# Optimization experiments

Measured on AMD Instinct MI355X. Metric: run time of the kernel, lower is better.

The kernel has to match this reference:

```python
import jax, jax.numpy as jnp
import numpy as np

C = 128      # input_dim
HEADS = 1    # inner_dim == input_dim (required by W_o channel counts)
INNER = C * HEADS
H = W = 80
EPS = 1e-5


def conv1x1(x, w, b):
    # x: [1,Cin,H,W], w: [Cout,Cin], b: [Cout]
    return jnp.einsum('bchw,oc->bohw', x, w) + b[None, :, None, None]


def bn_train(x, gamma, beta):
    # train-mode BatchNorm2d: per-channel stats over (B,H,W)
    mean = jnp.mean(x, axis=(0, 2, 3), keepdims=True)
    var = jnp.var(x, axis=(0, 2, 3), keepdims=True)
    xn = (x - mean) * jax.lax.rsqrt(var + EPS)
    return gamma[None, :, None, None] * xn + beta[None, :, None, None]


def proj(x, w, b, g, bt):
    return jax.nn.relu(bn_train(conv1x1(x, w, b), g, bt))


def setup_inputs() -> dict:
    key = jax.random.key(0)
    ks = jax.random.split(key, 12)
    d = {
        'query': jax.random.normal(ks[0], (1, C, H, W), jnp.float32),
        'key': jax.random.normal(ks[1], (1, C, H, W), jnp.float32),
        'value': jax.random.normal(ks[2], (1, C, H, W), jnp.float32),
        'pos_embedding': jax.random.normal(ks[3], (1, H, W), jnp.float32),
    }
    def lin(k, co, ci):
        return jax.random.normal(k, (co, ci), jnp.float32) * 0.02
    for name, k in zip(['q', 'k', 'v'], ks[4:7]):
        d['w' + name] = lin(k, INNER, C)
        d['b' + name] = jnp.zeros((INNER,), jnp.float32)
        d['g' + name] = jnp.ones((INNER,), jnp.float32)
        d['beta' + name] = jnp.zeros((INNER,), jnp.float32)
    d['wo1'] = lin(ks[7], C, INNER)
    d['bo1'] = jnp.zeros((C,), jnp.float32)
    d['go'] = jnp.ones((C,), jnp.float32)
    d['betao'] = jnp.zeros((C,), jnp.float32)
    d['wo2'] = lin(ks[8], C, INNER)
    d['bo2'] = jnp.zeros((C,), jnp.float32)
    return d


def reference(query, key, value, pos_embedding,
              wq, bq, gq, betaq,
              wk, bk, gk, betak,
              wv, bv, gv, betav,
              wo1, bo1, go, betao, wo2, bo2):
    dim = query.shape[1]
    q = proj(query, wq, bq, gq, betaq)   # [1,INNER,H,W]
    k = proj(key, wk, bk, gk, betak)
    v = proj(value, wv, bv, gv, betav)
    N = q.shape[2] * q.shape[3]
    # heads=1: rearrange 'b (c h) x y -> b h (x y) c' == flatten+transpose
    q2 = q.reshape(INNER, N).T           # [N, INNER]
    k2 = k.reshape(INNER, N).T
    v2 = v.reshape(INNER, N).T
    # pos context: pos repeated across all channels -> q2 @ ctx^T is an outer product
    pos = pos_embedding.reshape(N)
    ctx = jnp.sum(q2, axis=-1, keepdims=True) * pos[None, :]   # [N, N]
    score = (q2 @ k2.T) / jnp.sqrt(jnp.float32(dim)) + ctx
    attn = jax.nn.softmax(score, axis=-1)
    out = attn @ v2                      # [N, INNER]
    # buggy original rearrange: x = N, y = 1 -> spatial [N, 1]
    out = out.T.reshape(1, INNER, N, 1)
    h = jax.nn.relu(bn_train(conv1x1(out, wo1, bo1), go, betao))
    return conv1x1(h, wo2, bo2)          # [1, C, N, 1]
```

## Files before the change

### kernel.cpp

```cpp
#include <hip/hip_runtime.h>

#define NPIX 6400

typedef float f4 __attribute__((ext_vector_type(4)));
typedef float f16v __attribute__((ext_vector_type(16)));
typedef short bf16x8 __attribute__((ext_vector_type(8)));
typedef unsigned int u4 __attribute__((ext_vector_type(4)));
typedef unsigned int u2 __attribute__((ext_vector_type(2)));
typedef _Float16 h8 __attribute__((ext_vector_type(8)));
typedef _Float16 h4 __attribute__((ext_vector_type(4)));
typedef unsigned short u16;
typedef unsigned int u32;

__device__ __forceinline__ u16 f2bf(float f){
  union { float f; u32 u; } v; v.f = f;
  u32 r = v.u + 0x7fffu + ((v.u >> 16) & 1u);
  return (u16)(r >> 16);
}
__device__ __forceinline__ float bf2f(u16 h){
  union { u32 u; float f; } v; v.u = (u32)h << 16; return v.f;
}
__device__ __forceinline__ float exp2_hw(float x){ return __builtin_amdgcn_exp2f(x); }

__global__ __launch_bounds__(512, 1) void k_proj(
    const float* __restrict__ xq, const float* __restrict__ xk, const float* __restrict__ xv,
    const float* __restrict__ wq, const float* __restrict__ bq,
    const float* __restrict__ wk, const float* __restrict__ bk,
    const float* __restrict__ wv, const float* __restrict__ bv,
    u16* __restrict__ Y, float* __restrict__ psum, float* __restrict__ psq)
{
  __shared__ __align__(16) float wT[64][132];
  __shared__ __align__(16) float xt[64][132];
  __shared__ __align__(16) float red[2][16][128];
  const int bid = blockIdx.x;
  const int proj = bid / 50, pt = bid % 50;
  const float* x = (proj == 0) ? xq : ((proj == 1) ? xk : xv);
  const float* w = (proj == 0) ? wq : ((proj == 1) ? wk : wv);
  const float* b = (proj == 0) ? bq : ((proj == 1) ? bk : bv);
  const int t = threadIdx.x;
  const int o0 = (t & 31) * 4, p0 = (t >> 5) * 8;
  float acc[4][8];
  #pragma unroll
  for (int i = 0; i < 4; ++i)
    #pragma unroll
    for (int j = 0; j < 8; ++j) acc[i][j] = 0.f;
  for (int cc = 0; cc < 2; ++cc){
    __syncthreads();
    for (int idx = t; idx < 2048; idx += 512){
      int o = idx >> 4, c4 = (idx & 15) * 4;
      f4 wv4 = *(const f4*)&w[o * 128 + cc * 64 + c4];
      wT[c4 + 0][o] = wv4[0]; wT[c4 + 1][o] = wv4[1];
      wT[c4 + 2][o] = wv4[2]; wT[c4 + 3][o] = wv4[3];
    }
    for (int idx = t; idx < 2048; idx += 512){
      int c = idx >> 5, p4 = (idx & 31) * 4;
      *(f4*)&xt[c][p4] = *(const f4*)&x[(cc * 64 + c) * NPIX + pt * 128 + p4];
    }
    __syncthreads();
    for (int c = 0; c < 64; ++c){
      f4 w4 = *(const f4*)&wT[c][o0];
      f4 x0 = *(const f4*)&xt[c][p0];
      f4 x1 = *(const f4*)&xt[c][p0 + 4];
      #pragma unroll
      for (int i = 0; i < 4; ++i){
        float wi = w4[i];
        #pragma unroll
        for (int j = 0; j < 4; ++j){ acc[i][j] += wi * x0[j]; acc[i][4 + j] += wi * x1[j]; }
      }
    }
  }
  f4 b4 = *(const f4*)&b[o0];
  #pragma unroll
  for (int i = 0; i < 4; ++i)
    #pragma unroll
    for (int j = 0; j < 8; ++j) acc[i][j] += b4[i];
  #pragma unroll
  for (int i = 0; i < 4; ++i){
    float s = 0.f, q = 0.f;
    #pragma unroll
    for (int j = 0; j < 8; ++j){ s += acc[i][j]; q += acc[i][j] * acc[i][j]; }
    red[0][t >> 5][o0 + i] = s;
    red[1][t >> 5][o0 + i] = q;
  }
  __syncthreads();
  if (t < 128){
    float s = 0.f, q = 0.f;
    #pragma unroll
    for (int g = 0; g < 16; ++g){ s += red[0][g][t]; q += red[1][g][t]; }
    psum[(proj * 50 + pt) * 128 + t] = s;
    psq [(proj * 50 + pt) * 128 + t] = q;
  }
  u16* Yb = Y + (size_t)proj * NPIX * 128;
  if (proj < 2){
    #pragma unroll
    for (int j = 0; j < 8; ++j){
      u2 v;
      v[0] = (u32)f2bf(acc[0][j]) | ((u32)f2bf(acc[1][j]) << 16);
      v[1] = (u32)f2bf(acc[2][j]) | ((u32)f2bf(acc[3][j]) << 16);
      *(u2*)&Yb[(size_t)(pt * 128 + p0 + j) * 128 + o0] = v;
    }
  } else {
    #pragma unroll
    for (int i = 0; i < 4; ++i){
      u4 v;
      #pragma unroll
      for (int jj = 0; jj < 4; ++jj)
        v[jj] = (u32)f2bf(acc[i][jj * 2]) | ((u32)f2bf(acc[i][jj * 2 + 1]) << 16);
      *(u4*)&Yb[(size_t)(o0 + i) * NPIX + pt * 128 + p0] = v;
    }
  }
}

__global__ __launch_bounds__(512, 1) void k_norm(
    const u16* __restrict__ Y, const float* __restrict__ psum, const float* __restrict__ psq,
    const float* __restrict__ gq, const float* __restrict__ beq,
    const float* __restrict__ gk, const float* __restrict__ bek,
    const float* __restrict__ gv, const float* __restrict__ bev,
    u16* __restrict__ q2, u16* __restrict__ k2, u16* __restrict__ v2t,
    float* __restrict__ rowsumq)
{
  __shared__ float sc[128], sh[128];
  const int bid = blockIdx.x, t = threadIdx.x;
  const int proj = bid / 50, pt = bid % 50;
  if (t < 128){
    float s = 0.f, q = 0.f;
    for (int i = 0; i < 50; ++i){
      s += psum[(proj * 50 + i) * 128 + t];
      q += psq [(proj * 50 + i) * 128 + t];
    }
    float mean = s * (1.f / NPIX);
    float var  = q * (1.f / NPIX) - mean * mean;
    const float* g  = (proj == 0) ? gq : ((proj == 1) ? gk : gv);
    const float* be = (proj == 0) ? beq : ((proj == 1) ? bek : bev);
    float scale = g[t] * rsqrtf(var + 1e-5f);
    sc[t] = scale; sh[t] = be[t] - mean * scale;
  }
  __syncthreads();
  const u16* Yb = Y + (size_t)proj * NPIX * 128;
  if (proj < 2){
    int row = pt * 128 + (t >> 2), o0 = (t & 3) * 32;
    float rs = 0.f;
    u32 pkd[16];
    #pragma unroll
    for (int u = 0; u < 4; ++u){
      bf16x8 y8 = *(const bf16x8*)&Yb[(size_t)row * 128 + o0 + u * 8];
      #pragma unroll
      for (int e = 0; e < 8; ++e){
        int o = o0 + u * 8 + e;
        float v = fmaxf(bf2f((u16)y8[e]) * sc[o] + sh[o], 0.f);
        rs += v;
        if ((e & 1) == 0) pkd[u * 4 + (e >> 1)] = (u32)f2bf(v);
        else pkd[u * 4 + (e >> 1)] |= ((u32)f2bf(v) << 16);
      }
    }
    u16* dst = (proj == 0) ? q2 : k2;
    u4* dp = (u4*)(dst + (size_t)row * 128 + o0);
    #pragma unroll
    for (int u = 0; u < 4; ++u){
      u4 v; v[0] = pkd[u*4]; v[1] = pkd[u*4+1]; v[2] = pkd[u*4+2]; v[3] = pkd[u*4+3];
      dp[u] = v;
    }
    if (proj == 0){
      rs += __shfl_xor(rs, 1);
      rs += __shfl_xor(rs, 2);
      if ((t & 3) == 0) rowsumq[row] = rs;
    }
  } else {
    int o = t >> 2, pc = pt * 128 + (t & 3) * 32;
    float scale = sc[o], shift = sh[o];
    u32 pkd[16];
    #pragma unroll
    for (int u = 0; u < 4; ++u){
      bf16x8 y8 = *(const bf16x8*)&Yb[(size_t)o * NPIX + pc + u * 8];
      #pragma unroll
      for (int e = 0; e < 8; ++e){
        float v = fmaxf(bf2f((u16)y8[e]) * scale + shift, 0.f);
        if ((e & 1) == 0) pkd[u * 4 + (e >> 1)] = (u32)f2bf(v);
        else pkd[u * 4 + (e >> 1)] |= ((u32)f2bf(v) << 16);
      }
    }
    u4* dp = (u4*)(v2t + (size_t)o * NPIX + pc);
    #pragma unroll
    for (int u = 0; u < 4; ++u){
      u4 v; v[0] = pkd[u*4]; v[1] = pkd[u*4+1]; v[2] = pkd[u*4+2]; v[3] = pkd[u*4+3];
      dp[u] = v;
    }
  }
}

template<int NKT>
__global__ __launch_bounds__(512, 2) void k_flash(
    const u16* __restrict__ q2, const u16* __restrict__ k2, const u16* __restrict__ v2t,
    const float* __restrict__ rowsumq, const float* __restrict__ pos,
    _Float16* __restrict__ Opart, float* __restrict__ Mout, float* __restrict__ Lout,
    int js)
{
  __shared__ __align__(16) u16 Kt[2][64 * 128];
  __shared__ __align__(16) u16 Vt[2][128 * 64];
  __shared__ __align__(16) float posT[2][64];
  const int bid = blockIdx.x;
  const int qb = bid / js, jsi = bid % js;
  const int kt0 = jsi * NKT;
  const int tid = threadIdx.x;
  const int ln = tid & 63, wid = tid >> 6;
  const int lo = ln & 31, hi = ln >> 5;
  const int qrow = qb * 256 + wid * 32 + lo;

  const int kc_j = tid >> 4, kc_c8 = tid & 15;
  const int vc_d = tid >> 3, vc_c8 = tid & 7;
  bf16x8 kreg0, kreg1, vreg0, vreg1; float posr = 0.f;
  auto stage_load = [&](int j0){
    kreg0 = *(const bf16x8*)(k2 + (size_t)(j0 + kc_j) * 128 + kc_c8 * 8);
    kreg1 = *(const bf16x8*)(k2 + (size_t)(j0 + kc_j + 32) * 128 + kc_c8 * 8);
    vreg0 = *(const bf16x8*)(v2t + (size_t)vc_d * NPIX + j0 + vc_c8 * 8);
    vreg1 = *(const bf16x8*)(v2t + (size_t)(vc_d + 64) * NPIX + j0 + vc_c8 * 8);
    if (tid < 64) posr = pos[j0 + tid];
  };
  auto stage_write = [&](int b){
    char* kb = (char*)&Kt[b][0];
    char* vb = (char*)&Vt[b][0];
    *(bf16x8*)(kb + kc_j * 256 + ((kc_c8 * 16) ^ ((kc_j & 15) << 4))) = kreg0;
    *(bf16x8*)(kb + (kc_j + 32) * 256 + ((kc_c8 * 16) ^ (((kc_j + 32) & 15) << 4))) = kreg1;
    *(bf16x8*)(vb + vc_d * 128 + ((vc_c8 * 16) ^ ((vc_d & 7) << 4))) = vreg0;
    *(bf16x8*)(vb + (vc_d + 64) * 128 + ((vc_c8 * 16) ^ (((vc_d + 64) & 7) << 4))) = vreg1;
    if (tid < 64) posT[b][tid] = posr;
  };

  bf16x8 qf[8];
  const u16* qp = q2 + (size_t)qrow * 128 + hi * 8;
  #pragma unroll
  for (int kk = 0; kk < 8; ++kk) qf[kk] = *(const bf16x8*)(qp + kk * 16);
  const float rsq_l2 = rowsumq[qrow] * 1.4426950408889634f;
  f16v accO[4];
  #pragma unroll
  for (int c = 0; c < 4; ++c)
    #pragma unroll
    for (int r = 0; r < 16; ++r) accO[c][r] = 0.f;
  float m = -1e30f, l = 0.f;
  const float qs_l2 = 0.12751700f;

  stage_load(kt0 * 64);
  stage_write(0);
  __syncthreads();
  int cur = 0;

  #pragma unroll 2
  for (int kt = 0; kt < NKT; ++kt){
    const bool more = (kt + 1 < NKT);
    if (more) stage_load((kt0 + kt + 1) * 64);

    f16v aS0a, aS0b, aS1a, aS1b;
    #pragma unroll
    for (int r = 0; r < 16; ++r){ aS0a[r] = 0.f; aS0b[r] = 0.f; aS1a[r] = 0.f; aS1b[r] = 0.f; }
    {
      const char* kb0 = (const char*)&Kt[cur][0] + lo * 256;
      const char* kb1 = (const char*)&Kt[cur][0] + (32 + lo) * 256;
      const int sw = (lo & 15) << 4;
      #pragma unroll
      for (int kk = 0; kk < 4; ++kk){
        int boA = (kk * 32 + hi * 16) ^ sw;
        int boB = ((kk + 4) * 32 + hi * 16) ^ sw;
        bf16x8 kf0a = *(const bf16x8*)(kb0 + boA);
        bf16x8 kf1a = *(const bf16x8*)(kb1 + boA);
        bf16x8 kf0b = *(const bf16x8*)(kb0 + boB);
        bf16x8 kf1b = *(const bf16x8*)(kb1 + boB);
        aS0a = __builtin_amdgcn_mfma_f32_32x32x16_bf16(kf0a, qf[kk], aS0a, 0, 0, 0);
        aS1a = __builtin_amdgcn_mfma_f32_32x32x16_bf16(kf1a, qf[kk], aS1a, 0, 0, 0);
        aS0b = __builtin_amdgcn_mfma_f32_32x32x16_bf16(kf0b, qf[kk + 4], aS0b, 0, 0, 0);
        aS1b = __builtin_amdgcn_mfma_f32_32x32x16_bf16(kf1b, qf[kk + 4], aS1b, 0, 0, 0);
      }
    }
    float pv[32];
    float mx = -1e30f;
    #pragma unroll
    for (int jsb = 0; jsb < 2; ++jsb){
      #pragma unroll
      for (int g = 0; g < 4; ++g){
        f4 p4 = *(const f4*)&posT[cur][jsb * 32 + g * 8 + hi * 4];
        #pragma unroll
        for (int e = 0; e < 4; ++e){
          float sraw = jsb ? (aS1a[g * 4 + e] + aS1b[g * 4 + e])
                           : (aS0a[g * 4 + e] + aS0b[g * 4 + e]);
          float sv = sraw * qs_l2 + rsq_l2 * p4[e];
          pv[jsb * 16 + g * 4 + e] = sv;
          mx = fmaxf(mx, sv);
        }
      }
    }
    mx = fmaxf(mx, __shfl_xor(mx, 32));
    if (!__all(mx - m <= 11.5f)){
      float mnew = fmaxf(m, mx);
      float corr = exp2_hw(m - mnew);
      m = mnew;
      l *= corr;
      #pragma unroll
      for (int c = 0; c < 4; ++c)
        #pragma unroll
        for (int r = 0; r < 16; ++r) accO[c][r] *= corr;
    }
    float ls = 0.f;
    u32 pk[16];
    #pragma unroll
    for (int i = 0; i < 16; ++i){
      float e0 = exp2_hw(pv[2 * i]     - m);
      float e1 = exp2_hw(pv[2 * i + 1] - m);
      ls += e0 + e1;
      pk[i] = (u32)f2bf(e0) | ((u32)f2bf(e1) << 16);
    }
    ls += __shfl_xor(ls, 32);
    l += ls;

    if (more) stage_write(cur ^ 1);

    #pragma unroll
    for (int w = 0; w < 4; ++w){
      const int b0 = (w >> 1) * 8 + (w & 1) * 4;
      u32 s0 = __shfl_xor(pk[b0], 32);
      u32 s1 = __shfl_xor(pk[b0 + 1], 32);
      u32 s2 = __shfl_xor(pk[b0 + 2], 32);
      u32 s3 = __shfl_xor(pk[b0 + 3], 32);
      union { bf16x8 v; u32 u[4]; } pf;
      pf.u[0] = hi ? s2 : pk[b0];
      pf.u[1] = hi ? s3 : pk[b0 + 1];
      pf.u[2] = hi ? pk[b0 + 2] : s0;
      pf.u[3] = hi ? pk[b0 + 3] : s1;
      #pragma unroll
      for (int c = 0; c < 4; ++c){
        int d = c * 32 + lo;
        bf16x8 vf = *(const bf16x8*)((const char*)&Vt[cur][0] + d * 128 + ((w * 32 + hi * 16) ^ ((d & 7) << 4)));
        accO[c] = __builtin_amdgcn_mfma_f32_32x32x16_bf16(vf, pf.v, accO[c], 0, 0, 0);
      }
    }
    if (more) __syncthreads();
    cur ^= 1;
  }
  if (hi == 0){
    Mout[jsi * NPIX + qrow] = m;
    Lout[jsi * NPIX + qrow] = l;
  }
  const float linv = 1.f / l;
  _Float16* Ob = Opart + ((size_t)jsi * NPIX + qrow) * 128;
  #pragma unroll
  for (int c = 0; c < 4; ++c){
    #pragma unroll
    for (int g = 0; g < 4; ++g){
      h4 hv;
      #pragma unroll
      for (int e = 0; e < 4; ++e) hv[e] = (_Float16)(accO[c][g * 4 + e] * linv);
      *(h4*)&Ob[c * 32 + g * 8 + hi * 4] = hv;
    }
  }
}

template<int JS>
__global__ __launch_bounds__(256, 1) void k_out1(
    const _Float16* __restrict__ Opart, const float* __restrict__ Mbuf, const float* __restrict__ Lbuf,
    const float* __restrict__ wo1, const float* __restrict__ bo1,
    float* __restrict__ Z, float* __restrict__ p2s, float* __restrict__ p2q)
{
  __shared__ __align__(16) u16 wl[128 * 128];
  __shared__ __align__(16) u16 Ct[32 * 128];
  const int tid = threadIdx.x;
  {
    const int o = tid >> 1, h = tid & 1;
    const float* wp = wo1 + o * 128 + h * 64;
    char* dst = (char*)wl + o * 256;
    const int sw = (o & 15) << 4;
    #pragma unroll
    for (int u = 0; u < 8; ++u){
      f4 a = *(const f4*)(wp + u * 8);
      f4 b = *(const f4*)(wp + u * 8 + 4);
      union { bf16x8 v; u16 s[8]; } cc;
      #pragma unroll
      for (int e = 0; e < 4; ++e){ cc.s[e] = f2bf(a[e]); cc.s[4 + e] = f2bf(b[e]); }
      *(bf16x8*)(dst + ((h * 128 + u * 16) ^ sw)) = cc.v;
    }
  }
  {
    const int px = tid >> 3, c16 = (tid & 7) * 16;
    const int P = blockIdx.x * 32 + px;
    float coef[JS];
    float mmax = -1e30f;
    #pragma unroll
    for (int s = 0; s < JS; ++s){ coef[s] = Mbuf[s * NPIX + P]; mmax = fmaxf(mmax, coef[s]); }
    float den = 0.f;
    #pragma unroll
    for (int s = 0; s < JS; ++s){
      float w = exp2_hw(coef[s] - mmax) * Lbuf[s * NPIX + P];
      coef[s] = w; den += w;
    }
    float inv = 1.f / den;
    float a[16];
    #pragma unroll
    for (int e = 0; e < 16; ++e) a[e] = 0.f;
    #pragma unroll
    for (int s = 0; s < JS; ++s){
      float w = coef[s] * inv;
      const _Float16* op = Opart + ((size_t)s * NPIX + P) * 128 + c16;
      h8 h0 = *(const h8*)op;
      h8 h1 = *(const h8*)(op + 8);
      #pragma unroll
      for (int e = 0; e < 8; ++e){ a[e] += w * (float)h0[e]; a[8 + e] += w * (float)h1[e]; }
    }
    union { bf16x8 v; u16 s[8]; } c0, c1;
    #pragma unroll
    for (int e = 0; e < 8; ++e){ c0.s[e] = f2bf(a[e]); c1.s[e] = f2bf(a[8 + e]); }
    char* crow = (char*)Ct + px * 256;
    const int sw = (px & 15) << 4;
    *(bf16x8*)(crow + ((c16 * 2) ^ sw)) = c0.v;
    *(bf16x8*)(crow + ((c16 * 2 + 16) ^ sw)) = c1.v;
  }
  __syncthreads();
  const int ln = tid & 63, wid = tid >> 6, lo = ln & 31, hi = ln >> 5;
  const int p = blockIdx.x * 32 + lo;
  bf16x8 bfr[8];
  {
    const char* crow = (const char*)Ct + lo * 256;
    const int sw = (lo & 15) << 4;
    #pragma unroll
    for (int kk = 0; kk < 8; ++kk)
      bfr[kk] = *(const bf16x8*)(crow + ((kk * 32 + hi * 16) ^ sw));
  }
  f16v acc;
  #pragma unroll
  for (int r = 0; r < 16; ++r) acc[r] = 0.f;
  {
    const int o = wid * 32 + lo;
    const char* wrow = (const char*)wl + o * 256;
    const int sw = (o & 15) << 4;
    #pragma unroll
    for (int kk = 0; kk < 8; ++kk){
      bf16x8 wf = *(const bf16x8*)(wrow + ((kk * 32 + hi * 16) ^ sw));
      acc = __builtin_amdgcn_mfma_f32_32x32x16_bf16(wf, bfr[kk], acc, 0, 0, 0);
    }
  }
  #pragma unroll
  for (int g = 0; g < 4; ++g){
    const int o2 = wid * 32 + g * 8 + hi * 4;
    f4 b4 = *(const f4*)&bo1[o2];
    f4 zv;
    #pragma unroll
    for (int e = 0; e < 4; ++e) zv[e] = acc[g * 4 + e] + b4[e];
    *(f4*)&Z[(size_t)p * 128 + o2] = zv;
    #pragma unroll
    for (int e = 0; e < 4; ++e){
      float sv = zv[e], qv = zv[e] * zv[e];
      #pragma unroll
      for (int msk = 1; msk < 32; msk <<= 1){ sv += __shfl_xor(sv, msk); qv += __shfl_xor(qv, msk); }
      if (lo == 0){
        p2s[blockIdx.x * 128 + o2 + e] = sv;
        p2q[blockIdx.x * 128 + o2 + e] = qv;
      }
    }
  }
}

__global__ __launch_bounds__(256, 1) void k_out2(
    const float* __restrict__ Z, const float* __restrict__ p2s, const float* __restrict__ p2q,
    const float* __restrict__ go, const float* __restrict__ beo,
    const float* __restrict__ wo2, const float* __restrict__ bo2,
    float* __restrict__ out)
{
  __shared__ __align__(16) u16 wl[128 * 128];
  __shared__ float sc2[128], sh2[128];
  const int tid = threadIdx.x;
  if (tid < 128){
    float s = 0.f, q = 0.f;
    for (int i = 0; i < 200; ++i){ s += p2s[i * 128 + tid]; q += p2q[i * 128 + tid]; }
    float mean = s * (1.f / NPIX);
    float var  = q * (1.f / NPIX) - mean * mean;
    float scale = go[tid] * rsqrtf(var + 1e-5f);
    sc2[tid] = scale; sh2[tid] = beo[tid] - mean * scale;
  }
  {
    const int o = tid >> 1, h = tid & 1;
    const float* wp = wo2 + o * 128 + h * 64;
    char* dst = (char*)wl + o * 256;
    const int sw = (o & 15) << 4;
    #pragma unroll
    for (int u = 0; u < 8; ++u){
      f4 a = *(const f4*)(wp + u * 8);
      f4 b = *(const f4*)(wp + u * 8 + 4);
      union { bf16x8 v; u16 s[8]; } cc;
      #pragma unroll
      for (int e = 0; e < 4; ++e){ cc.s[e] = f2bf(a[e]); cc.s[4 + e] = f2bf(b[e]); }
      *(bf16x8*)(dst + ((h * 128 + u * 16) ^ sw)) = cc.v;
    }
  }
  __syncthreads();
  const int ln = tid & 63, wid = tid >> 6, lo = ln & 31, hi = ln >> 5;
  const int p = blockIdx.x * 128 + wid * 32 + lo;
  bf16x8 bfH[8];
  #pragma unroll
  for (int kk = 0; kk < 8; ++kk){
    int ob = kk * 16 + hi * 8;
    f4 z0 = *(const f4*)&Z[(size_t)p * 128 + ob];
    f4 z1 = *(const f4*)&Z[(size_t)p * 128 + ob + 4];
    f4 s0 = *(const f4*)&sc2[ob], s1 = *(const f4*)&sc2[ob + 4];
    f4 h0 = *(const f4*)&sh2[ob], h1 = *(const f4*)&sh2[ob + 4];
    union { bf16x8 v; u16 s[8]; } u;
    #pragma unroll
    for (int e = 0; e < 4; ++e){
      u.s[e]     = f2bf(fmaxf(z0[e] * s0[e] + h0[e], 0.f));
      u.s[4 + e] = f2bf(fmaxf(z1[e] * s1[e] + h1[e], 0.f));
    }
    bfH[kk] = u.v;
  }
  f16v acc[4];
  #pragma unroll
  for (int c = 0; c < 4; ++c)
    #pragma unroll
    for (int r = 0; r < 16; ++r) acc[c][r] = 0.f;
  #pragma unroll
  for (int c = 0; c < 4; ++c){
    const int o = c * 32 + lo;
    const char* wrow = (const char*)wl + o * 256;
    const int sw = (o & 15) << 4;
    #pragma unroll
    for (int kk = 0; kk < 8; ++kk){
      bf16x8 wf = *(const bf16x8*)(wrow + ((kk * 32 + hi * 16) ^ sw));
      acc[c] = __builtin_amdgcn_mfma_f32_32x32x16_bf16(wf, bfH[kk], acc[c], 0, 0, 0);
    }
  }
  #pragma unroll
  for (int c = 0; c < 4; ++c){
    #pragma unroll
    for (int g = 0; g < 4; ++g){
      const int o3 = c * 32 + g * 8 + hi * 4;
      f4 b4 = *(const f4*)&bo2[o3];
      #pragma unroll
      for (int e = 0; e < 4; ++e)
        out[(size_t)(o3 + e) * NPIX + p] = acc[c][g * 4 + e] + b4[e];
    }
  }
}

extern "C" void kernel_launch(void* const* d_in, const int* in_sizes, int n_in,
                              void* d_out, int out_size, void* d_ws, size_t ws_size,
                              hipStream_t stream)
{
  const float* query = (const float*)d_in[0];
  const float* key_  = (const float*)d_in[1];
  const float* value = (const float*)d_in[2];
  const float* pos   = (const float*)d_in[3];
  const float* wq = (const float*)d_in[4];  const float* bq = (const float*)d_in[5];
  const float* gq = (const float*)d_in[6];  const float* betaq = (const float*)d_in[7];
  const float* wk = (const float*)d_in[8];  const float* bk = (const float*)d_in[9];
  const float* gk = (const float*)d_in[10]; const float* betak = (const float*)d_in[11];
  const float* wv = (const float*)d_in[12]; const float* bv = (const float*)d_in[13];
  const float* gv = (const float*)d_in[14]; const float* betav = (const float*)d_in[15];
  const float* wo1 = (const float*)d_in[16]; const float* bo1 = (const float*)d_in[17];
  const float* go  = (const float*)d_in[18]; const float* betao = (const float*)d_in[19];
  const float* wo2 = (const float*)d_in[20]; const float* bo2 = (const float*)d_in[21];

  const size_t fixed = 8576000;
  auto need = [&](int j) -> size_t {
    size_t ml = (size_t)j * 51200;
    size_t op = (size_t)j * 1638400;
    size_t ov = op > 4915200 ? op : (size_t)4915200;
    return fixed + ml + ov;
  };
  int js = 5;
  if (ws_size >= need(10)) js = 10;

  char* W = (char*)d_ws;
  size_t off = 0;
  auto alloc = [&](size_t n){ char* p = W + off; off += n; return p; };
  u16*  q2      = (u16*)alloc(1638400);
  u16*  k2      = (u16*)alloc(1638400);
  u16*  v2t     = (u16*)alloc(1638400);
  float* rowsumq= (float*)alloc(25600);
  float* psum   = (float*)alloc(76800);
  float* psq    = (float*)alloc(76800);
  float* Z      = (float*)alloc(3276800);
  float* p2s    = (float*)alloc(102400);
  float* p2q    = (float*)alloc(102400);
  float* Mbuf   = (float*)alloc((size_t)js * 25600);
  float* Lbuf   = (float*)alloc((size_t)js * 25600);
  u16*  Y       = (u16*)(W + off);
  _Float16* Opart = (_Float16*)(W + off);

  k_proj <<<dim3(150), dim3(512), 0, stream>>>(query, key_, value, wq, bq, wk, bk, wv, bv, Y, psum, psq);
  k_norm <<<dim3(150), dim3(512), 0, stream>>>(Y, psum, psq, gq, betaq, gk, betak, gv, betav, q2, k2, v2t, rowsumq);
  if (js == 10){
    k_flash<10><<<dim3(25 * 10), dim3(512), 0, stream>>>(q2, k2, v2t, rowsumq, pos, Opart, Mbuf, Lbuf, 10);
    k_out1<10><<<dim3(200), dim3(256), 0, stream>>>(Opart, Mbuf, Lbuf, wo1, bo1, Z, p2s, p2q);
  } else {
    k_flash<20><<<dim3(25 * 5), dim3(512), 0, stream>>>(q2, k2, v2t, rowsumq, pos, Opart, Mbuf, Lbuf, 5);
    k_out1<5><<<dim3(200), dim3(256), 0, stream>>>(Opart, Mbuf, Lbuf, wo1, bo1, Z, p2s, p2q);
  }
  k_out2 <<<dim3(50), dim3(256), 0, stream>>>(Z, p2s, p2q, go, betao, wo2, bo2, (float*)d_out);
}
```

Baseline: 92.60 us.

## Double grid sizes for projection, norm and output kernels; fold Q scaling into norm

The projection and normalization kernels now cover 64 pixels per block instead of 128, doubling their grids to 300 blocks. The partial-statistics buffers grow to match. The softmax scale and log2(e) factors are folded into the stored Q values and row sums in k_norm, which removes a multiply per score in the flash kernel. k_out2 now handles 32 pixels per block across 200 blocks: each wave computes one 32-output slice and reads the normalized activations staged in a swizzled LDS tile. The goal is to fill more of the CUs on the small kernels, in exchange for more duplicated weight loads and more partial sums to reduce. Pre-scaling Q before bf16 rounding also slightly changes the numerics.

```diff
diff --git a/kernel.cpp b/kernel.cpp
--- a/kernel.cpp
+++ b/kernel.cpp
@@ -30,20 +30,20 @@
     u16* __restrict__ Y, float* __restrict__ psum, float* __restrict__ psq)
 {
   __shared__ __align__(16) float wT[64][132];
-  __shared__ __align__(16) float xt[64][132];
+  __shared__ __align__(16) float xt[64][68];
   __shared__ __align__(16) float red[2][16][128];
   const int bid = blockIdx.x;
-  const int proj = bid / 50, pt = bid % 50;
+  const int proj = bid / 100, pt = bid % 100;
   const float* x = (proj == 0) ? xq : ((proj == 1) ? xk : xv);
   const float* w = (proj == 0) ? wq : ((proj == 1) ? wk : wv);
   const float* b = (proj == 0) ? bq : ((proj == 1) ? bk : bv);
   const int t = threadIdx.x;
-  const int o0 = (t & 31) * 4, p0 = (t >> 5) * 8;
-  float acc[4][8];
+  const int o0 = (t & 31) * 4, p0 = (t >> 5) * 4;
+  float acc[4][4];
   #pragma unroll
   for (int i = 0; i < 4; ++i)
     #pragma unroll
-    for (int j = 0; j < 8; ++j) acc[i][j] = 0.f;
+    for (int j = 0; j < 4; ++j) acc[i][j] = 0.f;
   for (int cc = 0; cc < 2; ++cc){
     __syncthreads();
     for (int idx = t; idx < 2048; idx += 512){
@@ -52,20 +52,19 @@
       wT[c4 + 0][o] = wv4[0]; wT[c4 + 1][o] = wv4[1];
       wT[c4 + 2][o] = wv4[2]; wT[c4 + 3][o] = wv4[3];
     }
-    for (int idx = t; idx < 2048; idx += 512){
-      int c = idx >> 5, p4 = (idx & 31) * 4;
-      *(f4*)&xt[c][p4] = *(const f4*)&x[(cc * 64 + c) * NPIX + pt * 128 + p4];
+    for (int idx = t; idx < 1024; idx += 512){
+      int c = idx >> 4, p4 = (idx & 15) * 4;
+      *(f4*)&xt[c][p4] = *(const f4*)&x[(cc * 64 + c) * NPIX + pt * 64 + p4];
     }
     __syncthreads();
     for (int c = 0; c < 64; ++c){
       f4 w4 = *(const f4*)&wT[c][o0];
       f4 x0 = *(const f4*)&xt[c][p0];
-      f4 x1 = *(const f4*)&xt[c][p0 + 4];
       #pragma unroll
       for (int i = 0; i < 4; ++i){
         float wi = w4[i];
         #pragma unroll
-        for (int j = 0; j < 4; ++j){ acc[i][j] += wi * x0[j]; acc[i][4 + j] += wi * x1[j]; }
+        for (int j = 0; j < 4; ++j) acc[i][j] += wi * x0[j];
       }
     }
   }
@@ -73,12 +72,12 @@
   #pragma unroll
   for (int i = 0; i < 4; ++i)
     #pragma unroll
-    for (int j = 0; j < 8; ++j) acc[i][j] += b4[i];
+    for (int j = 0; j < 4; ++j) acc[i][j] += b4[i];
   #pragma unroll
   for (int i = 0; i < 4; ++i){
     float s = 0.f, q = 0.f;
     #pragma unroll
-    for (int j = 0; j < 8; ++j){ s += acc[i][j]; q += acc[i][j] * acc[i][j]; }
+    for (int j = 0; j < 4; ++j){ s += acc[i][j]; q += acc[i][j] * acc[i][j]; }
     red[0][t >> 5][o0 + i] = s;
     red[1][t >> 5][o0 + i] = q;
   }
@@ -87,26 +86,25 @@
     float s = 0.f, q = 0.f;
     #pragma unroll
     for (int g = 0; g < 16; ++g){ s += red[0][g][t]; q += red[1][g][t]; }
-    psum[(proj * 50 + pt) * 128 + t] = s;
-    psq [(proj * 50 + pt) * 128 + t] = q;
+    psum[(proj * 100 + pt) * 128 + t] = s;
+    psq [(proj * 100 + pt) * 128 + t] = q;
   }
   u16* Yb = Y + (size_t)proj * NPIX * 128;
   if (proj < 2){
     #pragma unroll
-    for (int j = 0; j < 8; ++j){
+    for (int j = 0; j < 4; ++j){
       u2 v;
       v[0] = (u32)f2bf(acc[0][j]) | ((u32)f2bf(acc[1][j]) << 16);
       v[1] = (u32)f2bf(acc[2][j]) | ((u32)f2bf(acc[3][j]) << 16);
-      *(u2*)&Yb[(size_t)(pt * 128 + p0 + j) * 128 + o0] = v;
+      *(u2*)&Yb[(size_t)(pt * 64 + p0 + j) * 128 + o0] = v;
     }
   } else {
     #pragma unroll
     for (int i = 0; i < 4; ++i){
-      u4 v;
-      #pragma unroll
-      for (int jj = 0; jj < 4; ++jj)
-        v[jj] = (u32)f2bf(acc[i][jj * 2]) | ((u32)f2bf(acc[i][jj * 2 + 1]) << 16);
-      *(u4*)&Yb[(size_t)(o0 + i) * NPIX + pt * 128 + p0] = v;
+      u2 v;
+      v[0] = (u32)f2bf(acc[i][0]) | ((u32)f2bf(acc[i][1]) << 16);
+      v[1] = (u32)f2bf(acc[i][2]) | ((u32)f2bf(acc[i][3]) << 16);
+      *(u2*)&Yb[(size_t)(o0 + i) * NPIX + pt * 64 + p0] = v;
     }
   }
 }
@@ -121,12 +119,12 @@
 {
   __shared__ float sc[128], sh[128];
   const int bid = blockIdx.x, t = threadIdx.x;
-  const int proj = bid / 50, pt = bid % 50;
+  const int proj = bid / 100, pt = bid % 100;
   if (t < 128){
     float s = 0.f, q = 0.f;
-    for (int i = 0; i < 50; ++i){
-      s += psum[(proj * 50 + i) * 128 + t];
-      q += psq [(proj * 50 + i) * 128 + t];
+    for (int i = 0; i < 100; ++i){
+      s += psum[(proj * 100 + i) * 128 + t];
+      q += psq [(proj * 100 + i) * 128 + t];
     }
     float mean = s * (1.f / NPIX);
     float var  = q * (1.f / NPIX) - mean * mean;
@@ -137,40 +135,44 @@
   }
   __syncthreads();
   const u16* Yb = Y + (size_t)proj * NPIX * 128;
+  const float qs_l2 = 0.12751700f;
   if (proj < 2){
-    int row = pt * 128 + (t >> 2), o0 = (t & 3) * 32;
+    const int row = pt * 64 + (t >> 3), o0 = (t & 7) * 16;
+    const float oscale = (proj == 0) ? qs_l2 : 1.f;
     float rs = 0.f;
-    u32 pkd[16];
-    #pragma unroll
-    for (int u = 0; u < 4; ++u){
+    u32 pkd[8];
+    #pragma unroll
+    for (int u = 0; u < 2; ++u){
       bf16x8 y8 = *(const bf16x8*)&Yb[(size_t)row * 128 + o0 + u * 8];
       #pragma unroll
       for (int e = 0; e < 8; ++e){
         int o = o0 + u * 8 + e;
         float v = fmaxf(bf2f((u16)y8[e]) * sc[o] + sh[o], 0.f);
         rs += v;
-        if ((e & 1) == 0) pkd[u * 4 + (e >> 1)] = (u32)f2bf(v);
-        else pkd[u * 4 + (e >> 1)] |= ((u32)f2bf(v) << 16);
+        float ov = v * oscale;
+        if ((e & 1) == 0) pkd[u * 4 + (e >> 1)] = (u32)f2bf(ov);
+        else pkd[u * 4 + (e >> 1)] |= ((u32)f2bf(ov) << 16);
       }
     }
     u16* dst = (proj == 0) ? q2 : k2;
     u4* dp = (u4*)(dst + (size_t)row * 128 + o0);
     #pragma unroll
-    for (int u = 0; u < 4; ++u){
+    for (int u = 0; u < 2; ++u){
       u4 v; v[0] = pkd[u*4]; v[1] = pkd[u*4+1]; v[2] = pkd[u*4+2]; v[3] = pkd[u*4+3];
       dp[u] = v;
     }
     if (proj == 0){
       rs += __shfl_xor(rs, 1);
       rs += __shfl_xor(rs, 2);
-      if ((t & 3) == 0) rowsumq[row] = rs;
+      rs += __shfl_xor(rs, 4);
+      if ((t & 7) == 0) rowsumq[row] = rs * 1.4426950408889634f;
     }
   } else {
-    int o = t >> 2, pc = pt * 128 + (t & 3) * 32;
+    const int o = t >> 2, pc = pt * 64 + (t & 3) * 16;
     float scale = sc[o], shift = sh[o];
-    u32 pkd[16];
-    #pragma unroll
-    for (int u = 0; u < 4; ++u){
+    u32 pkd[8];
+    #pragma unroll
+    for (int u = 0; u < 2; ++u){
       bf16x8 y8 = *(const bf16x8*)&Yb[(size_t)o * NPIX + pc + u * 8];
       #pragma unroll
       for (int e = 0; e < 8; ++e){
@@ -181,7 +183,7 @@
     }
     u4* dp = (u4*)(v2t + (size_t)o * NPIX + pc);
     #pragma unroll
-    for (int u = 0; u < 4; ++u){
+    for (int u = 0; u < 2; ++u){
       u4 v; v[0] = pkd[u*4]; v[1] = pkd[u*4+1]; v[2] = pkd[u*4+2]; v[3] = pkd[u*4+3];
       dp[u] = v;
     }
@@ -230,14 +232,13 @@
   const u16* qp = q2 + (size_t)qrow * 128 + hi * 8;
   #pragma unroll
   for (int kk = 0; kk < 8; ++kk) qf[kk] = *(const bf16x8*)(qp + kk * 16);
-  const float rsq_l2 = rowsumq[qrow] * 1.4426950408889634f;
+  const float rsq_l2 = rowsumq[qrow];
   f16v accO[4];
   #pragma unroll
   for (int c = 0; c < 4; ++c)
     #pragma unroll
     for (int r = 0; r < 16; ++r) accO[c][r] = 0.f;
   float m = -1e30f, l = 0.f;
-  const float qs_l2 = 0.12751700f;
 
   stage_load(kt0 * 64);
   stage_write(0);
@@ -281,7 +282,7 @@
         for (int e = 0; e < 4; ++e){
           float sraw = jsb ? (aS1a[g * 4 + e] + aS1b[g * 4 + e])
                            : (aS0a[g * 4 + e] + aS0b[g * 4 + e]);
-          float sv = sraw * qs_l2 + rsq_l2 * p4[e];
+          float sv = sraw + rsq_l2 * p4[e];
           pv[jsb * 16 + g * 4 + e] = sv;
           mx = fmaxf(mx, sv);
         }
@@ -462,6 +463,7 @@
     float* __restrict__ out)
 {
   __shared__ __align__(16) u16 wl[128 * 128];
+  __shared__ __align__(16) u16 Ct[32 * 128];
   __shared__ float sc2[128], sh2[128];
   const int tid = threadIdx.x;
   if (tid < 128){
@@ -488,50 +490,57 @@
     }
   }
   __syncthreads();
+  {
+    const int px = tid >> 3, c16 = (tid & 7) * 16;
+    const int P = blockIdx.x * 32 + px;
+    union { bf16x8 v; u16 s[8]; } c0, c1;
+    #pragma unroll
+    for (int u = 0; u < 4; ++u){
+      f4 z = *(const f4*)&Z[(size_t)P * 128 + c16 + u * 4];
+      f4 s4 = *(const f4*)&sc2[c16 + u * 4];
+      f4 h4v = *(const f4*)&sh2[c16 + u * 4];
+      #pragma unroll
+      for (int e = 0; e < 4; ++e){
+        u16 hb = f2bf(fmaxf(z[e] * s4[e] + h4v[e], 0.f));
+        if (u < 2) c0.s[u * 4 + e] = hb; else c1.s[(u - 2) * 4 + e] = hb;
+      }
+    }
+    char* crow = (char*)Ct + px * 256;
+    const int sw = (px & 15) << 4;
+    *(bf16x8*)(crow + ((c16 * 2) ^ sw)) = c0.v;
+    *(bf16x8*)(crow + ((c16 * 2 + 16) ^ sw)) = c1.v;
+  }
+  __syncthreads();
   const int ln = tid & 63, wid = tid >> 6, lo = ln & 31, hi = ln >> 5;
-  const int p = blockIdx.x * 128 + wid * 32 + lo;
+  const int p = blockIdx.x * 32 + lo;
   bf16x8 bfH[8];
-  #pragma unroll
-  for (int kk = 0; kk < 8; ++kk){
-    int ob = kk * 16 + hi * 8;
-    f4 z0 = *(const f4*)&Z[(size_t)p * 128 + ob];
-    f4 z1 = *(const f4*)&Z[(size_t)p * 128 + ob + 4];
-    f4 s0 = *(const f4*)&sc2[ob], s1 = *(const f4*)&sc2[ob + 4];
-    f4 h0 = *(const f4*)&sh2[ob], h1 = *(const f4*)&sh2[ob + 4];
-    union { bf16x8 v; u16 s[8]; } u;
-    #pragma unroll
-    for (int e = 0; e < 4; ++e){
-      u.s[e]     = f2bf(fmaxf(z0[e] * s0[e] + h0[e], 0.f));
-      u.s[4 + e] = f2bf(fmaxf(z1[e] * s1[e] + h1[e], 0.f));
-    }
-    bfH[kk] = u.v;
-  }
-  f16v acc[4];
-  #pragma unroll
-  for (int c = 0; c < 4; ++c)
-    #pragma unroll
-    for (int r = 0; r < 16; ++r) acc[c][r] = 0.f;
-  #pragma unroll
-  for (int c = 0; c < 4; ++c){
-    const int o = c * 32 + lo;
+  {
+    const char* crow = (const char*)Ct + lo * 256;
+    const int sw = (lo & 15) << 4;
+    #pragma unroll
+    for (int kk = 0; kk < 8; ++kk)
+      bfH[kk] = *(const bf16x8*)(crow + ((kk * 32 + hi * 16) ^ sw));
+  }
+  f16v acc;
+  #pragma unroll
+  for (int r = 0; r < 16; ++r) acc[r] = 0.f;
+  {
+    const int o = wid * 32 + lo;
     const char* wrow = (const char*)wl + o * 256;
     const int sw = (o & 15) << 4;
     #pragma unroll
     for (int kk = 0; kk < 8; ++kk){
       bf16x8 wf = *(const bf16x8*)(wrow + ((kk * 32 + hi * 16) ^ sw));
-      acc[c] = __builtin_amdgcn_mfma_f32_32x32x16_bf16(wf, bfH[kk], acc[c], 0, 0, 0);
-    }
-  }
-  #pragma unroll
-  for (int c = 0; c < 4; ++c){
-    #pragma unroll
-    for (int g = 0; g < 4; ++g){
-      const int o3 = c * 32 + g * 8 + hi * 4;
-      f4 b4 = *(const f4*)&bo2[o3];
-      #pragma unroll
-      for (int e = 0; e < 4; ++e)
-        out[(size_t)(o3 + e) * NPIX + p] = acc[c][g * 4 + e] + b4[e];
-    }
+      acc = __builtin_amdgcn_mfma_f32_32x32x16_bf16(wf, bfH[kk], acc, 0, 0, 0);
+    }
+  }
+  #pragma unroll
+  for (int g = 0; g < 4; ++g){
+    const int o3 = wid * 32 + g * 8 + hi * 4;
+    f4 b4 = *(const f4*)&bo2[o3];
+    #pragma unroll
+    for (int e = 0; e < 4; ++e)
+      out[(size_t)(o3 + e) * NPIX + p] = acc[g * 4 + e] + b4[e];
   }
 }
 
@@ -553,7 +562,7 @@
   const float* go  = (const float*)d_in[18]; const float* betao = (const float*)d_in[19];
   const float* wo2 = (const float*)d_in[20]; const float* bo2 = (const float*)d_in[21];
 
-  const size_t fixed = 8576000;
+  const size_t fixed = 8729600;
   auto need = [&](int j) -> size_t {
     size_t ml = (size_t)j * 51200;
     size_t op = (size_t)j * 1638400;
@@ -570,8 +579,8 @@
   u16*  k2      = (u16*)alloc(1638400);
   u16*  v2t     = (u16*)alloc(1638400);
   float* rowsumq= (float*)alloc(25600);
-  float* psum   = (float*)alloc(76800);
-  float* psq    = (float*)alloc(76800);
+  float* psum   = (float*)alloc(153600);
+  float* psq    = (float*)alloc(153600);
   float* Z      = (float*)alloc(3276800);
   float* p2s    = (float*)alloc(102400);
   float* p2q    = (float*)alloc(102400);
@@ -580,8 +589,8 @@
   u16*  Y       = (u16*)(W + off);
   _Float16* Opart = (_Float16*)(W + off);
 
-  k_proj <<<dim3(150), dim3(512), 0, stream>>>(query, key_, value, wq, bq, wk, bk, wv, bv, Y, psum, psq);
-  k_norm <<<dim3(150), dim3(512), 0, stream>>>(Y, psum, psq, gq, betaq, gk, betak, gv, betav, q2, k2, v2t, rowsumq);
+  k_proj <<<dim3(300), dim3(512), 0, stream>>>(query, key_, value, wq, bq, wk, bk, wv, bv, Y, psum, psq);
+  k_norm <<<dim3(300), dim3(512), 0, stream>>>(Y, psum, psq, gq, betaq, gk, betak, gv, betav, q2, k2, v2t, rowsumq);
   if (js == 10){
     k_flash<10><<<dim3(25 * 10), dim3(512), 0, stream>>>(q2, k2, v2t, rowsumq, pos, Opart, Mbuf, Lbuf, 10);
     k_out1<10><<<dim3(200), dim3(256), 0, stream>>>(Opart, Mbuf, Lbuf, wo1, bo1, Z, p2s, p2q);
@@ -589,5 +598,5 @@
     k_flash<20><<<dim3(25 * 5), dim3(512), 0, stream>>>(q2, k2, v2t, rowsumq, pos, Opart, Mbuf, Lbuf, 5);
     k_out1<5><<<dim3(200), dim3(256), 0, stream>>>(Opart, Mbuf, Lbuf, wo1, bo1, Z, p2s, p2q);
   }
-  k_out2 <<<dim3(50), dim3(256), 0, stream>>>(Z, p2s, p2q, go, betao, wo2, bo2, (float*)d_out);
-}
+  k_out2 <<<dim3(200), dim3(256), 0, stream>>>(Z, p2s, p2q, go, betao, wo2, bo2, (float*)d_out);
+}
```

New measurement: 167.0 us. +80.4%, slower.

## Fold softmax scale into q projection and split out2 across more blocks

Applied to the files above, without the earlier changes.

The 1/sqrt(d)·log2e scale is now applied to q when it is normalized and stored, and log2e is folded into rowsumq, which removes a multiply per score element in the flash inner loop. The final output kernel is restructured to run on 200 blocks of 32 pixels instead of 50 blocks of 128. Each block stages the normalized bf16 activations once in shared memory, and each wave computes one 32-channel output slice. This raises parallelism in the tail kernel, but every block still recomputes the BN stats and reloads the full weight matrix. Pre-scaling q before the bf16 rounding slightly changes numerics.

```diff
diff --git a/kernel.cpp b/kernel.cpp
--- a/kernel.cpp
+++ b/kernel.cpp
@@ -137,8 +137,10 @@
   }
   __syncthreads();
   const u16* Yb = Y + (size_t)proj * NPIX * 128;
+  const float qs_l2 = 0.12751700f;
   if (proj < 2){
     int row = pt * 128 + (t >> 2), o0 = (t & 3) * 32;
+    const float oscale = (proj == 0) ? qs_l2 : 1.f;
     float rs = 0.f;
     u32 pkd[16];
     #pragma unroll
@@ -149,8 +151,9 @@
         int o = o0 + u * 8 + e;
         float v = fmaxf(bf2f((u16)y8[e]) * sc[o] + sh[o], 0.f);
         rs += v;
-        if ((e & 1) == 0) pkd[u * 4 + (e >> 1)] = (u32)f2bf(v);
-        else pkd[u * 4 + (e >> 1)] |= ((u32)f2bf(v) << 16);
+        float ov = v * oscale;
+        if ((e & 1) == 0) pkd[u * 4 + (e >> 1)] = (u32)f2bf(ov);
+        else pkd[u * 4 + (e >> 1)] |= ((u32)f2bf(ov) << 16);
       }
     }
     u16* dst = (proj == 0) ? q2 : k2;
@@ -163,7 +166,7 @@
     if (proj == 0){
       rs += __shfl_xor(rs, 1);
       rs += __shfl_xor(rs, 2);
-      if ((t & 3) == 0) rowsumq[row] = rs;
+      if ((t & 3) == 0) rowsumq[row] = rs * 1.4426950408889634f;
     }
   } else {
     int o = t >> 2, pc = pt * 128 + (t & 3) * 32;
@@ -230,14 +233,13 @@
   const u16* qp = q2 + (size_t)qrow * 128 + hi * 8;
   #pragma unroll
   for (int kk = 0; kk < 8; ++kk) qf[kk] = *(const bf16x8*)(qp + kk * 16);
-  const float rsq_l2 = rowsumq[qrow] * 1.4426950408889634f;
+  const float rsq_l2 = rowsumq[qrow];
   f16v accO[4];
   #pragma unroll
   for (int c = 0; c < 4; ++c)
     #pragma unroll
     for (int r = 0; r < 16; ++r) accO[c][r] = 0.f;
   float m = -1e30f, l = 0.f;
-  const float qs_l2 = 0.12751700f;
 
   stage_load(kt0 * 64);
   stage_write(0);
@@ -281,7 +283,7 @@
         for (int e = 0; e < 4; ++e){
           float sraw = jsb ? (aS1a[g * 4 + e] + aS1b[g * 4 + e])
                            : (aS0a[g * 4 + e] + aS0b[g * 4 + e]);
-          float sv = sraw * qs_l2 + rsq_l2 * p4[e];
+          float sv = sraw + rsq_l2 * p4[e];
           pv[jsb * 16 + g * 4 + e] = sv;
           mx = fmaxf(mx, sv);
         }
@@ -462,6 +464,7 @@
     float* __restrict__ out)
 {
   __shared__ __align__(16) u16 wl[128 * 128];
+  __shared__ __align__(16) u16 Ct[32 * 128];
   __shared__ float sc2[128], sh2[128];
   const int tid = threadIdx.x;
   if (tid < 128){
@@ -488,50 +491,57 @@
     }
   }
   __syncthreads();
+  {
+    const int px = tid >> 3, c16 = (tid & 7) * 16;
+    const int P = blockIdx.x * 32 + px;
+    union { bf16x8 v; u16 s[8]; } c0, c1;
+    #pragma unroll
+    for (int u = 0; u < 4; ++u){
+      f4 z = *(const f4*)&Z[(size_t)P * 128 + c16 + u * 4];
+      f4 s4 = *(const f4*)&sc2[c16 + u * 4];
+      f4 h4v = *(const f4*)&sh2[c16 + u * 4];
+      #pragma unroll
+      for (int e = 0; e < 4; ++e){
+        u16 hb = f2bf(fmaxf(z[e] * s4[e] + h4v[e], 0.f));
+        if (u < 2) c0.s[u * 4 + e] = hb; else c1.s[(u - 2) * 4 + e] = hb;
+      }
+    }
+    char* crow = (char*)Ct + px * 256;
+    const int sw = (px & 15) << 4;
+    *(bf16x8*)(crow + ((c16 * 2) ^ sw)) = c0.v;
+    *(bf16x8*)(crow + ((c16 * 2 + 16) ^ sw)) = c1.v;
+  }
+  __syncthreads();
   const int ln = tid & 63, wid = tid >> 6, lo = ln & 31, hi = ln >> 5;
-  const int p = blockIdx.x * 128 + wid * 32 + lo;
+  const int p = blockIdx.x * 32 + lo;
   bf16x8 bfH[8];
-  #pragma unroll
-  for (int kk = 0; kk < 8; ++kk){
-    int ob = kk * 16 + hi * 8;
-    f4 z0 = *(const f4*)&Z[(size_t)p * 128 + ob];
-    f4 z1 = *(const f4*)&Z[(size_t)p * 128 + ob + 4];
-    f4 s0 = *(const f4*)&sc2[ob], s1 = *(const f4*)&sc2[ob + 4];
-    f4 h0 = *(const f4*)&sh2[ob], h1 = *(const f4*)&sh2[ob + 4];
-    union { bf16x8 v; u16 s[8]; } u;
-    #pragma unroll
-    for (int e = 0; e < 4; ++e){
-      u.s[e]     = f2bf(fmaxf(z0[e] * s0[e] + h0[e], 0.f));
-      u.s[4 + e] = f2bf(fmaxf(z1[e] * s1[e] + h1[e], 0.f));
-    }
-    bfH[kk] = u.v;
-  }
-  f16v acc[4];
-  #pragma unroll
-  for (int c = 0; c < 4; ++c)
-    #pragma unroll
-    for (int r = 0; r < 16; ++r) acc[c][r] = 0.f;
-  #pragma unroll
-  for (int c = 0; c < 4; ++c){
-    const int o = c * 32 + lo;
+  {
+    const char* crow = (const char*)Ct + lo * 256;
+    const int sw = (lo & 15) << 4;
+    #pragma unroll
+    for (int kk = 0; kk < 8; ++kk)
+      bfH[kk] = *(const bf16x8*)(crow + ((kk * 32 + hi * 16) ^ sw));
+  }
+  f16v acc;
+  #pragma unroll
+  for (int r = 0; r < 16; ++r) acc[r] = 0.f;
+  {
+    const int o = wid * 32 + lo;
     const char* wrow = (const char*)wl + o * 256;
     const int sw = (o & 15) << 4;
     #pragma unroll
     for (int kk = 0; kk < 8; ++kk){
       bf16x8 wf = *(const bf16x8*)(wrow + ((kk * 32 + hi * 16) ^ sw));
-      acc[c] = __builtin_amdgcn_mfma_f32_32x32x16_bf16(wf, bfH[kk], acc[c], 0, 0, 0);
-    }
-  }
-  #pragma unroll
-  for (int c = 0; c < 4; ++c){
-    #pragma unroll
-    for (int g = 0; g < 4; ++g){
-      const int o3 = c * 32 + g * 8 + hi * 4;
-      f4 b4 = *(const f4*)&bo2[o3];
-      #pragma unroll
-      for (int e = 0; e < 4; ++e)
-        out[(size_t)(o3 + e) * NPIX + p] = acc[c][g * 4 + e] + b4[e];
-    }
+      acc = __builtin_amdgcn_mfma_f32_32x32x16_bf16(wf, bfH[kk], acc, 0, 0, 0);
+    }
+  }
+  #pragma unroll
+  for (int g = 0; g < 4; ++g){
+    const int o3 = wid * 32 + g * 8 + hi * 4;
+    f4 b4 = *(const f4*)&bo2[o3];
+    #pragma unroll
+    for (int e = 0; e < 4; ++e)
+      out[(size_t)(o3 + e) * NPIX + p] = acc[g * 4 + e] + b4[e];
   }
 }
 
@@ -589,5 +599,5 @@
     k_flash<20><<<dim3(25 * 5), dim3(512), 0, stream>>>(q2, k2, v2t, rowsumq, pos, Opart, Mbuf, Lbuf, 5);
     k_out1<5><<<dim3(200), dim3(256), 0, stream>>>(Opart, Mbuf, Lbuf, wo1, bo1, Z, p2s, p2q);
   }
-  k_out2 <<<dim3(50), dim3(256), 0, stream>>>(Z, p2s, p2q, go, betao, wo2, bo2, (float*)d_out);
-}
+  k_out2 <<<dim3(200), dim3(256), 0, stream>>>(Z, p2s, p2q, go, betao, wo2, bo2, (float*)d_out);
+}
```

Measured after the change: 87.43 us. 5.6% less time.
